# Optimization experiments

Hardware: AMD Instinct MI355X
Metric: run time of the kernel (lower is better)

The kernel has to match this reference:

```python
import jax, jax.numpy as jnp
import numpy as np

D_IN = 2048
D_OUT = 2048
NUM_HEADS = 16
NUM_KV_GROUPS = 4
GROUP_SIZE = NUM_HEADS // NUM_KV_GROUPS  # 4
HEAD_DIM = D_OUT // NUM_HEADS            # 128


def setup_inputs() -> dict:
    key = jax.random.key(0)
    ks = jax.random.split(key, 6)
    b, n = 2, 2048
    x = jax.random.normal(ks[0], (b, n, D_IN), dtype=jnp.float32)
    # weights stored as [in, out] so that x @ W matches torch's x @ weight.T
    Wq = jax.random.normal(ks[1], (D_IN, D_OUT), dtype=jnp.float32) * (1.0 / np.sqrt(D_IN))
    Wk = jax.random.normal(ks[2], (D_IN, NUM_KV_GROUPS * HEAD_DIM), dtype=jnp.float32) * (1.0 / np.sqrt(D_IN))
    Wv = jax.random.normal(ks[3], (D_IN, NUM_KV_GROUPS * HEAD_DIM), dtype=jnp.float32) * (1.0 / np.sqrt(D_IN))
    Wo = jax.random.normal(ks[4], (D_OUT, D_OUT), dtype=jnp.float32) * (1.0 / np.sqrt(D_OUT))
    bo = jax.random.normal(ks[5], (D_OUT,), dtype=jnp.float32) * 0.01
    return {"x": x, "Wq": Wq, "Wk": Wk, "Wv": Wv, "Wo": Wo, "bo": bo}


def reference(x, Wq, Wk, Wv, Wo, bo):
    b, n, _ = x.shape
    # projections
    q = (x @ Wq).reshape(b, n, NUM_KV_GROUPS, GROUP_SIZE, HEAD_DIM)  # [b,n,g,s,d]
    k = (x @ Wk).reshape(b, n, NUM_KV_GROUPS, HEAD_DIM)              # [b,n,g,d]
    v = (x @ Wv).reshape(b, n, NUM_KV_GROUPS, HEAD_DIM)
    scale = 1.0 / np.sqrt(HEAD_DIM).astype(np.float32)
    # scores: each group of GROUP_SIZE query heads shares one K/V head
    scores = jnp.einsum('bqgsd,bkgd->bgsqk', q, k) * scale  # [b,g,s,n,n]
    causal = jnp.arange(n)[:, None] < jnp.arange(n)[None, :]  # True above diagonal
    scores = jnp.where(causal, -jnp.inf, scores)
    attn = jax.nn.softmax(scores, axis=-1)
    # dropout omitted for determinism (eval-mode equivalent)
    ctx = jnp.einsum('bgsqk,bkgd->bqgsd', attn, v)  # [b,n,g,s,d]
    ctx = ctx.reshape(b, n, D_OUT)
    return ctx @ Wo + bo
```

## Files before the change

kernel.cpp:

```cpp
#include <hip/hip_runtime.h>
#include <hip/hip_bf16.h>

typedef short bf16x8 __attribute__((ext_vector_type(8)));
typedef float f32x4 __attribute__((ext_vector_type(4)));
typedef float f32x16 __attribute__((ext_vector_type(16)));
typedef unsigned int u32x4 __attribute__((ext_vector_type(4)));

#define MFMA16(a, b, c) __builtin_amdgcn_mfma_f32_16x16x32_bf16((a), (b), (c), 0, 0, 0)
#define MFMA32(a, b, c) __builtin_amdgcn_mfma_f32_32x32x16_bf16((a), (b), (c), 0, 0, 0)

static __device__ __forceinline__ unsigned short f2bf(float f) {
  union { float f; unsigned u; } v;
  v.f = f;
  unsigned r = (v.u + 0x7FFFu + ((v.u >> 16) & 1u)) >> 16;
  return (unsigned short)r;
}

static __device__ __forceinline__ unsigned pk2(float a, float b) {
  unsigned ua = __float_as_uint(a) + 0x8000u;
  unsigned ub = __float_as_uint(b) + 0x8000u;
  return (ua >> 16) | (ub & 0xFFFF0000u);
}

static __device__ __forceinline__ void gload16(const void* g, void* l) {
  __builtin_amdgcn_global_load_lds(
      (const __attribute__((address_space(1))) unsigned int*)g,
      (__attribute__((address_space(3))) unsigned int*)l, 16, 0, 0);
}

__global__ __launch_bounds__(256) void cast_f32_bf16(
    const float* __restrict__ src, unsigned short* __restrict__ dst, int n4) {
  int stride = gridDim.x * blockDim.x;
  for (int i = blockIdx.x * blockDim.x + threadIdx.x; i < n4; i += stride) {
    float4 v = reinterpret_cast<const float4*>(src)[i];
    ushort4 o;
    o.x = f2bf(v.x); o.y = f2bf(v.y); o.z = f2bf(v.z); o.w = f2bf(v.w);
    reinterpret_cast<ushort4*>(dst)[i] = o;
  }
}

__global__ __launch_bounds__(256) void prep_all(
    const float* __restrict__ Wq, const float* __restrict__ Wk,
    const float* __restrict__ Wv, const float* __restrict__ Wo,
    unsigned short* __restrict__ WqT, unsigned short* __restrict__ WkT,
    unsigned short* __restrict__ WvT, unsigned short* __restrict__ WoT) {
  __shared__ float tile[32][33];
  int id = blockIdx.x;
  const float* src; unsigned short* dst; int R, C, bx, by;
  if (id < 4096)      { src = Wq; dst = WqT; R = 2048; C = 2048; bx = id & 63; by = id >> 6; }
  else if (id < 5120) { id -= 4096; src = Wk; dst = WkT; R = 2048; C = 512; bx = id & 15; by = id >> 4; }
  else if (id < 6144) { id -= 5120; src = Wv; dst = WvT; R = 2048; C = 512; bx = id & 15; by = id >> 4; }
  else                { id -= 6144; src = Wo; dst = WoT; R = 2048; C = 2048; bx = id & 63; by = id >> 6; }
  int tx = threadIdx.x & 31;
  int ty = threadIdx.x >> 5;
  int r0 = by * 32, c0 = bx * 32;
#pragma unroll
  for (int i = 0; i < 32; i += 8)
    tile[ty + i][tx] = src[(size_t)(r0 + ty + i) * C + (c0 + tx)];
  __syncthreads();
#pragma unroll
  for (int i = 0; i < 32; i += 8)
    dst[(size_t)(c0 + ty + i) * R + (r0 + tx)] = f2bf(tile[tx][ty + i]);
}

template <int EPI>
static __device__ __forceinline__ void g8p_core(
    const unsigned short* __restrict__ A, const unsigned short* __restrict__ B,
    unsigned short* __restrict__ Cb, unsigned short* __restrict__ Cb2,
    float* __restrict__ Cf, const float* __restrict__ bias,
    int N, int K, int bid, unsigned short* Al, unsigned short* Bl) {
  const int tid = threadIdx.x;
  const int wave = tid >> 6, lane = tid & 63;
  const int l15 = lane & 15, l4 = lane >> 4;
  const int tilesN = N >> 7;
  const int bm = bid / tilesN, bn = bid % tilesN;
  const int row0 = bm << 8, col0 = bn << 7;
  const int wr = (wave >> 1) << 6;
  const int wc = (wave & 1) << 6;

  const unsigned short* sA[4];
  const unsigned short* sB[2];
#pragma unroll
  for (int i = 0; i < 4; ++i) {
    int q = i * 512 + wave * 64 + lane;
    int r = q >> 3, c = (q & 7) ^ (r & 7);
    sA[i] = A + (size_t)(row0 + r) * K + c * 8;
  }
#pragma unroll
  for (int i = 0; i < 2; ++i) {
    int q = i * 512 + wave * 64 + lane;
    int r = q >> 3, c = (q & 7) ^ (r & 7);
    sB[i] = B + (size_t)(col0 + r) * K + c * 8;
  }

#define STG_H1(t_, bi)                                                      \
  { const size_t ko = (size_t)(t_) * 64;                                    \
    gload16(sA[0] + ko, &Al[(bi)*16384 + (0 * 512 + wave * 64) * 8]);       \
    gload16(sA[1] + ko, &Al[(bi)*16384 + (1 * 512 + wave * 64) * 8]);       \
    gload16(sB[0] + ko, &Bl[(bi)*8192 + (0 * 512 + wave * 64) * 8]); }
#define STG_H2(t_, bi)                                                      \
  { const size_t ko = (size_t)(t_) * 64;                                    \
    gload16(sA[2] + ko, &Al[(bi)*16384 + (2 * 512 + wave * 64) * 8]);       \
    gload16(sA[3] + ko, &Al[(bi)*16384 + (3 * 512 + wave * 64) * 8]);       \
    gload16(sB[1] + ko, &Bl[(bi)*8192 + (1 * 512 + wave * 64) * 8]); }

  const int sw = l15 & 7;
  const int c0 = (l4 ^ sw) << 4;
  const int c1 = ((4 + l4) ^ sw) << 4;
  const int rbA = (wr + l15) << 7;
  const int rbB = (wc + l15) << 7;

  f32x4 acc[4][4] = {};
  const int NT = K >> 6;

  STG_H1(0, 0); STG_H2(0, 0);
  STG_H1(1, 1); STG_H2(1, 1);

  int cur = 0;
  for (int t = 0; t < NT; ++t) {
    int sb = cur + 2; if (sb >= 3) sb -= 3;
    if (t + 1 < NT) { asm volatile("s_waitcnt vmcnt(6)" ::: "memory"); }
    else            { asm volatile("s_waitcnt vmcnt(0)" ::: "memory"); }
    __builtin_amdgcn_s_barrier();
    asm volatile("" ::: "memory");
    const char* Ab = (const char*)&Al[cur * 16384];
    const char* Bb = (const char*)&Bl[cur * 8192];
    bf16x8 b0[4], b1[4], aA[2][2], aB[2][2];
#pragma unroll
    for (int n = 0; n < 4; ++n) {
      b0[n] = *(const bf16x8*)(Bb + rbB + n * 2048 + c0);
      b1[n] = *(const bf16x8*)(Bb + rbB + n * 2048 + c1);
    }
#pragma unroll
    for (int m = 0; m < 2; ++m) {
      aA[m][0] = *(const bf16x8*)(Ab + rbA + m * 2048 + c0);
      aA[m][1] = *(const bf16x8*)(Ab + rbA + m * 2048 + c1);
    }
    if (t + 2 < NT) STG_H1(t + 2, sb);
    asm volatile("" ::: "memory");
    __builtin_amdgcn_s_barrier();
    asm volatile("" ::: "memory");
    __builtin_amdgcn_s_setprio(1);
#pragma unroll
    for (int m = 0; m < 2; ++m)
#pragma unroll
      for (int n = 0; n < 4; ++n) {
        acc[m][n] = MFMA16(aA[m][0], b0[n], acc[m][n]);
        acc[m][n] = MFMA16(aA[m][1], b1[n], acc[m][n]);
      }
    __builtin_amdgcn_s_setprio(0);
#pragma unroll
    for (int m = 0; m < 2; ++m) {
      aB[m][0] = *(const bf16x8*)(Ab + rbA + (m + 2) * 2048 + c0);
      aB[m][1] = *(const bf16x8*)(Ab + rbA + (m + 2) * 2048 + c1);
    }
    if (t + 2 < NT) STG_H2(t + 2, sb);
    asm volatile("" ::: "memory");
    __builtin_amdgcn_s_barrier();
    asm volatile("" ::: "memory");
    __builtin_amdgcn_s_setprio(1);
#pragma unroll
    for (int m = 0; m < 2; ++m)
#pragma unroll
      for (int n = 0; n < 4; ++n) {
        acc[m + 2][n] = MFMA16(aB[m][0], b0[n], acc[m + 2][n]);
        acc[m + 2][n] = MFMA16(aB[m][1], b1[n], acc[m + 2][n]);
      }
    __builtin_amdgcn_s_setprio(0);
    cur += 1; if (cur >= 3) cur = 0;
  }
#undef STG_H1
#undef STG_H2

#pragma unroll
  for (int m = 0; m < 4; ++m) {
#pragma unroll
    for (int n = 0; n < 4; ++n) {
      int row = row0 + wr + m * 16 + l4 * 4;
      int col = col0 + wc + n * 16 + l15;
#pragma unroll
      for (int r = 0; r < 4; ++r) {
        if (EPI == 0) {
          Cb[(size_t)(row + r) * N + col] = f2bf(acc[m][n][r]);
        } else if (EPI == 1) {
          Cf[(size_t)(row + r) * N + col] = acc[m][n][r] + bias[col];
        } else {
          if (col < 2048) Cb[(size_t)(row + r) * 2048 + col] = f2bf(acc[m][n][r]);
          else            Cb2[(size_t)(row + r) * 512 + col - 2048] = f2bf(acc[m][n][r]);
        }
      }
    }
  }
}

__global__ __launch_bounds__(512, 2) void gemm8p_o(
    const unsigned short* __restrict__ A, const unsigned short* __restrict__ B,
    float* __restrict__ Cf, const float* __restrict__ bias, int N, int K) {
  __shared__ unsigned short Al[3 * 256 * 64];
  __shared__ unsigned short Bl[3 * 128 * 64];
  g8p_core<1>(A, B, nullptr, nullptr, Cf, bias, N, K, blockIdx.x, Al, Bl);
}

__global__ __launch_bounds__(512, 2) void gemm_fused3(
    const unsigned short* __restrict__ Xb, const unsigned short* __restrict__ Bqk,
    unsigned short* __restrict__ Qb, unsigned short* __restrict__ Kb,
    const unsigned short* __restrict__ WvT, unsigned short* __restrict__ VTb) {
  __shared__ unsigned short Al[3 * 256 * 64];
  __shared__ unsigned short Bl[3 * 128 * 64];
  if (blockIdx.x < 320)
    g8p_core<2>(Xb, Bqk, Qb, Kb, nullptr, nullptr, 2560, 2048, blockIdx.x, Al, Bl);
  else
    g8p_core<0>(WvT, Xb, VTb, nullptr, nullptr, nullptr, 4096, 2048, blockIdx.x - 320, Al, Bl);
}

__global__ __launch_bounds__(256, 2) void flash_gqa6(
    const unsigned short* __restrict__ Qb, const unsigned short* __restrict__ Kb,
    const unsigned short* __restrict__ VT, unsigned short* __restrict__ Ctx) {
  __shared__ unsigned short Sm[24576];

  const int tid = threadIdx.x;
  const int wave = tid >> 6, lane = tid & 63;
  const int l31 = lane & 31, hi = lane >> 5;
  const int i = blockIdx.x >> 3;
  const int bg = blockIdx.x & 7;
  const int qt = (i < 32) ? i : (95 - i);
  const int b = bg >> 2, g = bg & 3;
  const int h = (g << 2) | wave;
  const int q0 = qt << 5;
  const int T = qt + 1;

  bf16x8 qf[8];
  {
    const unsigned short* qp =
        Qb + (size_t)(b * 2048 + q0 + l31) * 2048 + h * 128 + hi * 8;
#pragma unroll
    for (int ds = 0; ds < 8; ++ds) qf[ds] = *(const bf16x8*)(qp + ds * 16);
  }

  const int rK0 = tid >> 4, cK = tid & 15, rK1 = rK0 + 16;
  const unsigned short* kSA =
      Kb + (size_t)(b * 2048 + rK0) * 512 + g * 128 + (cK ^ (rK0 & 7)) * 8;
  const unsigned short* kSB =
      Kb + (size_t)(b * 2048 + rK1) * 512 + g * 128 + (cK ^ (rK1 & 7)) * 8;
  const int cV = tid & 7;
  const unsigned short* vS[4];
#pragma unroll
  for (int c = 0; c < 4; ++c) {
    int row = c * 32 + (tid >> 3);
    vS[c] = VT + (size_t)(g * 128 + row) * 4096 + b * 2048 + (cV ^ (row & 7)) * 8;
  }

#define STAGE_K(t_, bi)                                           \
  {                                                               \
    unsigned short* kb_ = Sm + (bi)*4096;                         \
    const size_t ko_ = (size_t)(t_) * 32 * 512;                   \
    gload16(kSA + ko_, kb_ + wave * 512);                         \
    gload16(kSB + ko_, kb_ + 2048 + wave * 512);                  \
  }
#define STAGE_V(p_, bi, half)                                     \
  {                                                               \
    unsigned short* vb_ = Sm + 8192 + (bi)*8192;                  \
    const size_t po_ = (size_t)(p_) * 64;                         \
    const int c_ = (half)*2;                                      \
    gload16(vS[c_] + po_, vb_ + c_ * 2048 + wave * 512);          \
    gload16(vS[c_ + 1] + po_, vb_ + (c_ + 1) * 2048 + wave * 512);\
  }

  const float s2 = 0.12751744f;

  float m_r = -1e30f, l_r = 0.f;
  f32x16 o0 = {}, o1 = {}, o2 = {}, o3 = {};

  STAGE_K(0, 0);
  STAGE_V(0, 0, 0);
  STAGE_V(0, 0, 1);
  __syncthreads();

  for (int t = 0; t < T; ++t) {
    const int buf = t & 1;
    const int pb = (t >> 1) & 1;
    if (t + 1 < T) STAGE_K(t + 1, buf ^ 1);
    const int p1 = (t >> 1) + 1;
    if (2 * p1 < T) STAGE_V(p1, p1 & 1, t & 1);

    const char* Kl = (const char*)Sm + buf * 8192;
    const char* Vl = (const char*)Sm + 16384 + pb * 16384;
    const int kv = t << 5;
    f32x16 st = {};
    __builtin_amdgcn_s_setprio(1);
#pragma unroll
    for (int ds = 0; ds < 8; ++ds) {
      const int by = (l31 * 256 + ds * 32 + hi * 16) ^ ((l31 & 7) << 4);
      bf16x8 kf = *(const bf16x8*)(Kl + by);
      st = MFMA32(kf, qf[ds], st);
    }
    __builtin_amdgcn_s_setprio(0);
    if (t == qt) {
      const int q_abs = q0 + l31;
#pragma unroll
      for (int rr = 0; rr < 16; ++rr) {
        const int koff = (rr & 3) + 8 * (rr >> 2) + 4 * hi;
        st[rr] = (kv + koff <= q_abs) ? st[rr] * s2 : -1e30f;
      }
    } else {
#pragma unroll
      for (int rr = 0; rr < 16; ++rr) st[rr] *= s2;
    }
    float pm = st[0];
#pragma unroll
    for (int rr = 1; rr < 16; ++rr) pm = fmaxf(pm, st[rr]);
    pm = fmaxf(pm, __shfl_xor(pm, 32));
    if (!__all(pm - m_r <= 11.5f)) {
      const float mn = fmaxf(m_r, pm);
      const float osc = exp2f(m_r - mn);
      m_r = mn;
      l_r *= osc;
#pragma unroll
      for (int rr = 0; rr < 16; ++rr) {
        o0[rr] *= osc; o1[rr] *= osc; o2[rr] *= osc; o3[rr] *= osc;
      }
    }
    float ps = 0.f;
#pragma unroll
    for (int rr = 0; rr < 16; ++rr) { st[rr] = exp2f(st[rr] - m_r); ps += st[rr]; }
    ps += __shfl_xor(ps, 32);
    l_r += ps;
    unsigned w[8];
#pragma unroll
    for (int rp = 0; rp < 8; ++rp) w[rp] = pk2(st[2 * rp], st[2 * rp + 1]);
    __builtin_amdgcn_s_setprio(1);
#define PV_KS(ks)                                                             \
    {                                                                         \
      const int k4 = (ks)*4;                                                  \
      unsigned a0 = w[k4], a1 = w[k4 + 1], b0 = w[k4 + 2], b1 = w[k4 + 3];    \
      unsigned q0_ = hi ? a0 : b0, q1_ = hi ? a1 : b1;                        \
      unsigned e0 = (unsigned)__shfl_xor((int)q0_, 32);                       \
      unsigned e1 = (unsigned)__shfl_xor((int)q1_, 32);                       \
      union { u32x4 u; bf16x8 v; } pk;                                        \
      pk.u[0] = hi ? e0 : a0; pk.u[1] = hi ? e1 : a1;                         \
      pk.u[2] = hi ? b0 : e0; pk.u[3] = hi ? b1 : e1;                         \
      const int cb = (t & 1) * 64 + (ks)*32 + hi * 16;                        \
      { const int row = l31;      const int by = (row * 128 + cb) ^ ((row & 7) << 4); \
        bf16x8 vf = *(const bf16x8*)(Vl + by); o0 = MFMA32(vf, pk.v, o0); }   \
      { const int row = 32 + l31; const int by = (row * 128 + cb) ^ ((row & 7) << 4); \
        bf16x8 vf = *(const bf16x8*)(Vl + by); o1 = MFMA32(vf, pk.v, o1); }   \
      { const int row = 64 + l31; const int by = (row * 128 + cb) ^ ((row & 7) << 4); \
        bf16x8 vf = *(const bf16x8*)(Vl + by); o2 = MFMA32(vf, pk.v, o2); }   \
      { const int row = 96 + l31; const int by = (row * 128 + cb) ^ ((row & 7) << 4); \
        bf16x8 vf = *(const bf16x8*)(Vl + by); o3 = MFMA32(vf, pk.v, o3); }   \
    }
    PV_KS(0) PV_KS(1)
#undef PV_KS
    __builtin_amdgcn_s_setprio(0);
    __syncthreads();
  }
#undef STAGE_K
#undef STAGE_V

  const float inv = 1.f / l_r;
  unsigned short* cp = Ctx + (size_t)(b * 2048 + q0 + l31) * 2048 + h * 128;
#pragma unroll
  for (int a = 0; a < 4; ++a) {
    ushort4 p0, p1, p2, p3;
    p0.x = f2bf(o0[4 * a + 0] * inv); p0.y = f2bf(o0[4 * a + 1] * inv);
    p0.z = f2bf(o0[4 * a + 2] * inv); p0.w = f2bf(o0[4 * a + 3] * inv);
    p1.x = f2bf(o1[4 * a + 0] * inv); p1.y = f2bf(o1[4 * a + 1] * inv);
    p1.z = f2bf(o1[4 * a + 2] * inv); p1.w = f2bf(o1[4 * a + 3] * inv);
    p2.x = f2bf(o2[4 * a + 0] * inv); p2.y = f2bf(o2[4 * a + 1] * inv);
    p2.z = f2bf(o2[4 * a + 2] * inv); p2.w = f2bf(o2[4 * a + 3] * inv);
    p3.x = f2bf(o3[4 * a + 0] * inv); p3.y = f2bf(o3[4 * a + 1] * inv);
    p3.z = f2bf(o3[4 * a + 2] * inv); p3.w = f2bf(o3[4 * a + 3] * inv);
    const int cc = 8 * a + 4 * hi;
    *(ushort4*)(cp + 0 * 32 + cc) = p0;
    *(ushort4*)(cp + 1 * 32 + cc) = p1;
    *(ushort4*)(cp + 2 * 32 + cc) = p2;
    *(ushort4*)(cp + 3 * 32 + cc) = p3;
  }
}

extern "C" void kernel_launch(void* const* d_in, const int* in_sizes, int n_in,
                              void* d_out, int out_size, void* d_ws, size_t ws_size,
                              hipStream_t stream) {
  (void)in_sizes; (void)n_in; (void)out_size; (void)ws_size;
  const float* x  = (const float*)d_in[0];
  const float* Wq = (const float*)d_in[1];
  const float* Wk = (const float*)d_in[2];
  const float* Wv = (const float*)d_in[3];
  const float* Wo = (const float*)d_in[4];
  const float* bo = (const float*)d_in[5];
  float* out = (float*)d_out;

  unsigned short* Xb  = (unsigned short*)d_ws;
  unsigned short* WqT = Xb  + (size_t)4096 * 2048;
  unsigned short* WkT = WqT + (size_t)2048 * 2048;
  unsigned short* WvT = WkT + (size_t)512 * 2048;
  unsigned short* WoT = WvT + (size_t)512 * 2048;
  unsigned short* Qb  = WoT + (size_t)2048 * 2048;
  unsigned short* Kb  = Qb  + (size_t)4096 * 2048;
  unsigned short* VTb = Kb  + (size_t)4096 * 512;
  unsigned short* Ctx = VTb + (size_t)512 * 4096;

  cast_f32_bf16<<<2048, 256, 0, stream>>>(x, Xb, (4096 * 2048) / 4);
  prep_all<<<10240, 256, 0, stream>>>(Wq, Wk, Wv, Wo, WqT, WkT, WvT, WoT);

  gemm_fused3<<<dim3(384), 512, 0, stream>>>(Xb, WqT, Qb, Kb, WvT, VTb);

  flash_gqa6<<<dim3(512), 256, 0, stream>>>(Qb, Kb, VTb, Ctx);

  gemm8p_o<<<dim3(256), 512, 0, stream>>>(Ctx, WoT, out, bo, 2048, 2048);
}
```

Before: 209.8 us.

## Widen flash attention KV tile to 64 keys per iteration

The attention kernel now processes 64 keys per loop iteration instead of 32, staging K and V together into double-buffered LDS tiles of 64 rows. This halves the number of loop iterations, barriers and online-softmax rescale checks, and gives each iteration more independent MFMAs to overlap. In exchange LDS use grows from 48 KB to 64 KB per block, register pressure rises from the two score accumulators, and the diagonal tile may compute up to 32 fully masked keys.

```diff
diff --git a/kernel.cpp b/kernel.cpp
--- a/kernel.cpp
+++ b/kernel.cpp
@@ -213,10 +213,10 @@
     g8p_core<0>(WvT, Xb, VTb, nullptr, nullptr, nullptr, 4096, 2048, blockIdx.x - 320, Al, Bl);
 }
 
-__global__ __launch_bounds__(256, 2) void flash_gqa6(
+__global__ __launch_bounds__(256, 2) void flash_gqa7(
     const unsigned short* __restrict__ Qb, const unsigned short* __restrict__ Kb,
     const unsigned short* __restrict__ VT, unsigned short* __restrict__ Ctx) {
-  __shared__ unsigned short Sm[24576];
+  __shared__ unsigned short Sm[32768];
 
   const int tid = threadIdx.x;
   const int wave = tid >> 6, lane = tid & 63;
@@ -227,7 +227,7 @@
   const int b = bg >> 2, g = bg & 3;
   const int h = (g << 2) | wave;
   const int q0 = qt << 5;
-  const int T = qt + 1;
+  const int T = (qt >> 1) + 1;
 
   bf16x8 qf[8];
   {
@@ -237,78 +237,76 @@
     for (int ds = 0; ds < 8; ++ds) qf[ds] = *(const bf16x8*)(qp + ds * 16);
   }
 
-  const int rK0 = tid >> 4, cK = tid & 15, rK1 = rK0 + 16;
-  const unsigned short* kSA =
-      Kb + (size_t)(b * 2048 + rK0) * 512 + g * 128 + (cK ^ (rK0 & 7)) * 8;
-  const unsigned short* kSB =
-      Kb + (size_t)(b * 2048 + rK1) * 512 + g * 128 + (cK ^ (rK1 & 7)) * 8;
-  const int cV = tid & 7;
-  const unsigned short* vS[4];
-#pragma unroll
-  for (int c = 0; c < 4; ++c) {
-    int row = c * 32 + (tid >> 3);
-    vS[c] = VT + (size_t)(g * 128 + row) * 4096 + b * 2048 + (cV ^ (row & 7)) * 8;
-  }
-
-#define STAGE_K(t_, bi)                                           \
-  {                                                               \
-    unsigned short* kb_ = Sm + (bi)*4096;                         \
-    const size_t ko_ = (size_t)(t_) * 32 * 512;                   \
-    gload16(kSA + ko_, kb_ + wave * 512);                         \
-    gload16(kSB + ko_, kb_ + 2048 + wave * 512);                  \
-  }
-#define STAGE_V(p_, bi, half)                                     \
-  {                                                               \
-    unsigned short* vb_ = Sm + 8192 + (bi)*8192;                  \
-    const size_t po_ = (size_t)(p_) * 64;                         \
-    const int c_ = (half)*2;                                      \
-    gload16(vS[c_] + po_, vb_ + c_ * 2048 + wave * 512);          \
-    gload16(vS[c_ + 1] + po_, vb_ + (c_ + 1) * 2048 + wave * 512);\
+  const int cK = tid & 15, rK = tid >> 4;
+  const unsigned short* kS0 = Kb + (size_t)(b * 2048 + rK +  0) * 512 + g * 128 + (cK ^ ((rK +  0) & 7)) * 8;
+  const unsigned short* kS1 = Kb + (size_t)(b * 2048 + rK + 16) * 512 + g * 128 + (cK ^ ((rK + 16) & 7)) * 8;
+  const unsigned short* kS2 = Kb + (size_t)(b * 2048 + rK + 32) * 512 + g * 128 + (cK ^ ((rK + 32) & 7)) * 8;
+  const unsigned short* kS3 = Kb + (size_t)(b * 2048 + rK + 48) * 512 + g * 128 + (cK ^ ((rK + 48) & 7)) * 8;
+  const int cV = tid & 7, rV = tid >> 3;
+  const unsigned short* vS0 = VT + (size_t)(g * 128 + rV +  0) * 4096 + b * 2048 + (cV ^ ((rV +  0) & 7)) * 8;
+  const unsigned short* vS1 = VT + (size_t)(g * 128 + rV + 32) * 4096 + b * 2048 + (cV ^ ((rV + 32) & 7)) * 8;
+  const unsigned short* vS2 = VT + (size_t)(g * 128 + rV + 64) * 4096 + b * 2048 + (cV ^ ((rV + 64) & 7)) * 8;
+  const unsigned short* vS3 = VT + (size_t)(g * 128 + rV + 96) * 4096 + b * 2048 + (cV ^ ((rV + 96) & 7)) * 8;
+
+#define STAGE7(t_, bi)                                          \
+  {                                                             \
+    unsigned short* kb_ = Sm + (bi)*8192;                       \
+    unsigned short* vb_ = Sm + 16384 + (bi)*8192;               \
+    const size_t ko_ = (size_t)(t_) * 64 * 512;                 \
+    const size_t vo_ = (size_t)(t_) * 64;                       \
+    gload16(kS0 + ko_, kb_ + 0 * 2048 + wave * 512);            \
+    gload16(kS1 + ko_, kb_ + 1 * 2048 + wave * 512);            \
+    gload16(kS2 + ko_, kb_ + 2 * 2048 + wave * 512);            \
+    gload16(kS3 + ko_, kb_ + 3 * 2048 + wave * 512);            \
+    gload16(vS0 + vo_, vb_ + 0 * 2048 + wave * 512);            \
+    gload16(vS1 + vo_, vb_ + 1 * 2048 + wave * 512);            \
+    gload16(vS2 + vo_, vb_ + 2 * 2048 + wave * 512);            \
+    gload16(vS3 + vo_, vb_ + 3 * 2048 + wave * 512);            \
   }
 
   const float s2 = 0.12751744f;
-
   float m_r = -1e30f, l_r = 0.f;
   f32x16 o0 = {}, o1 = {}, o2 = {}, o3 = {};
 
-  STAGE_K(0, 0);
-  STAGE_V(0, 0, 0);
-  STAGE_V(0, 0, 1);
+  STAGE7(0, 0);
   __syncthreads();
 
   for (int t = 0; t < T; ++t) {
     const int buf = t & 1;
-    const int pb = (t >> 1) & 1;
-    if (t + 1 < T) STAGE_K(t + 1, buf ^ 1);
-    const int p1 = (t >> 1) + 1;
-    if (2 * p1 < T) STAGE_V(p1, p1 & 1, t & 1);
-
-    const char* Kl = (const char*)Sm + buf * 8192;
-    const char* Vl = (const char*)Sm + 16384 + pb * 16384;
-    const int kv = t << 5;
-    f32x16 st = {};
+    if (t + 1 < T) STAGE7(t + 1, buf ^ 1);
+    const char* Kl = (const char*)Sm + buf * 16384;
+    const char* Vl = (const char*)Sm + 32768 + buf * 16384;
+    const int kv = t << 6;
+    f32x16 st0 = {}, st1 = {};
     __builtin_amdgcn_s_setprio(1);
 #pragma unroll
     for (int ds = 0; ds < 8; ++ds) {
-      const int by = (l31 * 256 + ds * 32 + hi * 16) ^ ((l31 & 7) << 4);
-      bf16x8 kf = *(const bf16x8*)(Kl + by);
-      st = MFMA32(kf, qf[ds], st);
+      const int c = ds * 32 + hi * 16;
+      const int by0 = (l31 * 256 + c) ^ ((l31 & 7) << 4);
+      const int by1 = ((32 + l31) * 256 + c) ^ ((l31 & 7) << 4);
+      bf16x8 kf0 = *(const bf16x8*)(Kl + by0);
+      bf16x8 kf1 = *(const bf16x8*)(Kl + by1);
+      st0 = MFMA32(kf0, qf[ds], st0);
+      st1 = MFMA32(kf1, qf[ds], st1);
     }
     __builtin_amdgcn_s_setprio(0);
-    if (t == qt) {
-      const int q_abs = q0 + l31;
+    const int q_abs = q0 + l31;
+    if (kv + 64 > q0) {
 #pragma unroll
       for (int rr = 0; rr < 16; ++rr) {
         const int koff = (rr & 3) + 8 * (rr >> 2) + 4 * hi;
-        st[rr] = (kv + koff <= q_abs) ? st[rr] * s2 : -1e30f;
+        st0[rr] = (kv + koff <= q_abs) ? st0[rr] * s2 : -1e30f;
+        st1[rr] = (kv + 32 + koff <= q_abs) ? st1[rr] * s2 : -1e30f;
       }
     } else {
 #pragma unroll
-      for (int rr = 0; rr < 16; ++rr) st[rr] *= s2;
-    }
-    float pm = st[0];
-#pragma unroll
-    for (int rr = 1; rr < 16; ++rr) pm = fmaxf(pm, st[rr]);
+      for (int rr = 0; rr < 16; ++rr) { st0[rr] *= s2; st1[rr] *= s2; }
+    }
+    float pm = st0[0];
+#pragma unroll
+    for (int rr = 1; rr < 16; ++rr) pm = fmaxf(pm, st0[rr]);
+#pragma unroll
+    for (int rr = 0; rr < 16; ++rr) pm = fmaxf(pm, st1[rr]);
     pm = fmaxf(pm, __shfl_xor(pm, 32));
     if (!__all(pm - m_r <= 11.5f)) {
       const float mn = fmaxf(m_r, pm);
@@ -322,24 +320,29 @@
     }
     float ps = 0.f;
 #pragma unroll
-    for (int rr = 0; rr < 16; ++rr) { st[rr] = exp2f(st[rr] - m_r); ps += st[rr]; }
+    for (int rr = 0; rr < 16; ++rr) { st0[rr] = exp2f(st0[rr] - m_r); ps += st0[rr]; }
+#pragma unroll
+    for (int rr = 0; rr < 16; ++rr) { st1[rr] = exp2f(st1[rr] - m_r); ps += st1[rr]; }
     ps += __shfl_xor(ps, 32);
     l_r += ps;
-    unsigned w[8];
-#pragma unroll
-    for (int rp = 0; rp < 8; ++rp) w[rp] = pk2(st[2 * rp], st[2 * rp + 1]);
+    unsigned w0[8], w1[8];
+#pragma unroll
+    for (int rp = 0; rp < 8; ++rp) {
+      w0[rp] = pk2(st0[2 * rp], st0[2 * rp + 1]);
+      w1[rp] = pk2(st1[2 * rp], st1[2 * rp + 1]);
+    }
     __builtin_amdgcn_s_setprio(1);
-#define PV_KS(ks)                                                             \
+#define PV_KS(ks, W)                                                          \
     {                                                                         \
-      const int k4 = (ks)*4;                                                  \
-      unsigned a0 = w[k4], a1 = w[k4 + 1], b0 = w[k4 + 2], b1 = w[k4 + 3];    \
+      const int k4 = ((ks) & 1) * 4;                                          \
+      unsigned a0 = W[k4], a1 = W[k4 + 1], b0 = W[k4 + 2], b1 = W[k4 + 3];    \
       unsigned q0_ = hi ? a0 : b0, q1_ = hi ? a1 : b1;                        \
       unsigned e0 = (unsigned)__shfl_xor((int)q0_, 32);                       \
       unsigned e1 = (unsigned)__shfl_xor((int)q1_, 32);                       \
       union { u32x4 u; bf16x8 v; } pk;                                        \
       pk.u[0] = hi ? e0 : a0; pk.u[1] = hi ? e1 : a1;                         \
       pk.u[2] = hi ? b0 : e0; pk.u[3] = hi ? b1 : e1;                         \
-      const int cb = (t & 1) * 64 + (ks)*32 + hi * 16;                        \
+      const int cb = (ks)*32 + hi * 16;                                       \
       { const int row = l31;      const int by = (row * 128 + cb) ^ ((row & 7) << 4); \
         bf16x8 vf = *(const bf16x8*)(Vl + by); o0 = MFMA32(vf, pk.v, o0); }   \
       { const int row = 32 + l31; const int by = (row * 128 + cb) ^ ((row & 7) << 4); \
@@ -349,13 +352,12 @@
       { const int row = 96 + l31; const int by = (row * 128 + cb) ^ ((row & 7) << 4); \
         bf16x8 vf = *(const bf16x8*)(Vl + by); o3 = MFMA32(vf, pk.v, o3); }   \
     }
-    PV_KS(0) PV_KS(1)
+    PV_KS(0, w0) PV_KS(1, w0) PV_KS(2, w1) PV_KS(3, w1)
 #undef PV_KS
     __builtin_amdgcn_s_setprio(0);
     __syncthreads();
   }
-#undef STAGE_K
-#undef STAGE_V
+#undef STAGE7
 
   const float inv = 1.f / l_r;
   unsigned short* cp = Ctx + (size_t)(b * 2048 + q0 + l31) * 2048 + h * 128;
@@ -405,7 +407,7 @@
 
   gemm_fused3<<<dim3(384), 512, 0, stream>>>(Xb, WqT, Qb, Kb, WvT, VTb);
 
-  flash_gqa6<<<dim3(512), 256, 0, stream>>>(Qb, Kb, VTb, Ctx);
+  flash_gqa7<<<dim3(512), 256, 0, stream>>>(Qb, Kb, VTb, Ctx);
 
   gemm8p_o<<<dim3(256), 512, 0, stream>>>(Ctx, WoT, out, bo, 2048, 2048);
 }
```

After: 197.3 us. -5.9%, faster.

## Split KV range across two wave groups in flash attention with LDS merge

Applied to the files above, without the earlier changes.

The attention block grows from 4 to 8 waves. Each head now has two waves that handle alternating 32-key tiles (split-K over the KV sequence), and both stage a 64-key K/V chunk per iteration into a larger double-buffered shared memory. At the end, the second wave's partial output, max and sum go through LDS and are merged with the first wave's state using log-sum-exp rescaling. The goal is to halve the serial loop length per block and add more waves for latency hiding, at the cost of more LDS, a final merge step and idle waves on the odd tile of the diagonal.

```diff
diff --git a/kernel.cpp b/kernel.cpp
--- a/kernel.cpp
+++ b/kernel.cpp
@@ -213,10 +213,10 @@
     g8p_core<0>(WvT, Xb, VTb, nullptr, nullptr, nullptr, 4096, 2048, blockIdx.x - 320, Al, Bl);
 }
 
-__global__ __launch_bounds__(256, 2) void flash_gqa6(
+__global__ __launch_bounds__(512, 4) void flash_gqa8(
     const unsigned short* __restrict__ Qb, const unsigned short* __restrict__ Kb,
     const unsigned short* __restrict__ VT, unsigned short* __restrict__ Ctx) {
-  __shared__ unsigned short Sm[24576];
+  __shared__ unsigned short Sm[34816];
 
   const int tid = threadIdx.x;
   const int wave = tid >> 6, lane = tid & 63;
@@ -225,9 +225,11 @@
   const int bg = blockIdx.x & 7;
   const int qt = (i < 32) ? i : (95 - i);
   const int b = bg >> 2, g = bg & 3;
-  const int h = (g << 2) | wave;
+  const int hl = wave & 3;
+  const int h = (g << 2) | hl;
+  const int part = wave >> 2;
   const int q0 = qt << 5;
-  const int T = qt + 1;
+  const int R = (qt >> 1) + 1;
 
   bf16x8 qf[8];
   {
@@ -237,144 +239,169 @@
     for (int ds = 0; ds < 8; ++ds) qf[ds] = *(const bf16x8*)(qp + ds * 16);
   }
 
-  const int rK0 = tid >> 4, cK = tid & 15, rK1 = rK0 + 16;
-  const unsigned short* kSA =
-      Kb + (size_t)(b * 2048 + rK0) * 512 + g * 128 + (cK ^ (rK0 & 7)) * 8;
-  const unsigned short* kSB =
-      Kb + (size_t)(b * 2048 + rK1) * 512 + g * 128 + (cK ^ (rK1 & 7)) * 8;
-  const int cV = tid & 7;
-  const unsigned short* vS[4];
-#pragma unroll
-  for (int c = 0; c < 4; ++c) {
-    int row = c * 32 + (tid >> 3);
-    vS[c] = VT + (size_t)(g * 128 + row) * 4096 + b * 2048 + (cV ^ (row & 7)) * 8;
-  }
-
-#define STAGE_K(t_, bi)                                           \
-  {                                                               \
-    unsigned short* kb_ = Sm + (bi)*4096;                         \
-    const size_t ko_ = (size_t)(t_) * 32 * 512;                   \
-    gload16(kSA + ko_, kb_ + wave * 512);                         \
-    gload16(kSB + ko_, kb_ + 2048 + wave * 512);                  \
-  }
-#define STAGE_V(p_, bi, half)                                     \
-  {                                                               \
-    unsigned short* vb_ = Sm + 8192 + (bi)*8192;                  \
-    const size_t po_ = (size_t)(p_) * 64;                         \
-    const int c_ = (half)*2;                                      \
-    gload16(vS[c_] + po_, vb_ + c_ * 2048 + wave * 512);          \
-    gload16(vS[c_ + 1] + po_, vb_ + (c_ + 1) * 2048 + wave * 512);\
+  const int rK = tid >> 4, cK = tid & 15;
+  const unsigned short* kS =
+      Kb + (size_t)(b * 2048 + rK) * 512 + g * 128 + (cK ^ (rK & 7)) * 8;
+  const int rV = tid >> 3, cV = tid & 7;
+  const unsigned short* vSa =
+      VT + (size_t)(g * 128 + rV) * 4096 + b * 2048 + (cV ^ (rV & 7)) * 8;
+  const int rVb = rV + 64;
+  const unsigned short* vSb =
+      VT + (size_t)(g * 128 + rVb) * 4096 + b * 2048 + (cV ^ (rVb & 7)) * 8;
+
+#define STAGE8(r_, bi)                                                   \
+  {                                                                      \
+    unsigned short* base_ = Sm + (bi)*16384;                             \
+    const int t0_ = 2 * (r_);                                            \
+    gload16(kS + (size_t)t0_ * 16384, base_ + wave * 512);               \
+    if (t0_ + 1 <= qt)                                                   \
+      gload16(kS + (size_t)(t0_ + 1) * 16384, base_ + 4096 + wave * 512);\
+    const size_t vo_ = (size_t)(r_) * 64;                                \
+    gload16(vSa + vo_, base_ + 8192 + wave * 512);                       \
+    gload16(vSb + vo_, base_ + 12288 + wave * 512);                      \
   }
 
   const float s2 = 0.12751744f;
-
   float m_r = -1e30f, l_r = 0.f;
   f32x16 o0 = {}, o1 = {}, o2 = {}, o3 = {};
 
-  STAGE_K(0, 0);
-  STAGE_V(0, 0, 0);
-  STAGE_V(0, 0, 1);
+  STAGE8(0, 0);
   __syncthreads();
 
-  for (int t = 0; t < T; ++t) {
-    const int buf = t & 1;
-    const int pb = (t >> 1) & 1;
-    if (t + 1 < T) STAGE_K(t + 1, buf ^ 1);
-    const int p1 = (t >> 1) + 1;
-    if (2 * p1 < T) STAGE_V(p1, p1 & 1, t & 1);
-
-    const char* Kl = (const char*)Sm + buf * 8192;
-    const char* Vl = (const char*)Sm + 16384 + pb * 16384;
-    const int kv = t << 5;
-    f32x16 st = {};
-    __builtin_amdgcn_s_setprio(1);
-#pragma unroll
-    for (int ds = 0; ds < 8; ++ds) {
-      const int by = (l31 * 256 + ds * 32 + hi * 16) ^ ((l31 & 7) << 4);
-      bf16x8 kf = *(const bf16x8*)(Kl + by);
-      st = MFMA32(kf, qf[ds], st);
-    }
-    __builtin_amdgcn_s_setprio(0);
-    if (t == qt) {
-      const int q_abs = q0 + l31;
-#pragma unroll
-      for (int rr = 0; rr < 16; ++rr) {
-        const int koff = (rr & 3) + 8 * (rr >> 2) + 4 * hi;
-        st[rr] = (kv + koff <= q_abs) ? st[rr] * s2 : -1e30f;
-      }
-    } else {
-#pragma unroll
-      for (int rr = 0; rr < 16; ++rr) st[rr] *= s2;
-    }
-    float pm = st[0];
-#pragma unroll
-    for (int rr = 1; rr < 16; ++rr) pm = fmaxf(pm, st[rr]);
-    pm = fmaxf(pm, __shfl_xor(pm, 32));
-    if (!__all(pm - m_r <= 11.5f)) {
-      const float mn = fmaxf(m_r, pm);
-      const float osc = exp2f(m_r - mn);
-      m_r = mn;
-      l_r *= osc;
-#pragma unroll
-      for (int rr = 0; rr < 16; ++rr) {
-        o0[rr] *= osc; o1[rr] *= osc; o2[rr] *= osc; o3[rr] *= osc;
-      }
-    }
-    float ps = 0.f;
-#pragma unroll
-    for (int rr = 0; rr < 16; ++rr) { st[rr] = exp2f(st[rr] - m_r); ps += st[rr]; }
-    ps += __shfl_xor(ps, 32);
-    l_r += ps;
-    unsigned w[8];
-#pragma unroll
-    for (int rp = 0; rp < 8; ++rp) w[rp] = pk2(st[2 * rp], st[2 * rp + 1]);
-    __builtin_amdgcn_s_setprio(1);
+  for (int r = 0; r < R; ++r) {
+    const int buf = r & 1;
+    if (r + 1 < R) STAGE8(r + 1, buf ^ 1);
+    const int t32 = 2 * r + part;
+    if (t32 <= qt) {
+      const char* Kl = (const char*)Sm + buf * 32768 + part * 8192;
+      const char* Vl = (const char*)Sm + buf * 32768 + 16384;
+      const int kv = t32 << 5;
+      f32x16 st = {};
+      __builtin_amdgcn_s_setprio(1);
+#pragma unroll
+      for (int ds = 0; ds < 8; ++ds) {
+        const int by = (l31 * 256 + ds * 32 + hi * 16) ^ ((l31 & 7) << 4);
+        bf16x8 kf = *(const bf16x8*)(Kl + by);
+        st = MFMA32(kf, qf[ds], st);
+      }
+      __builtin_amdgcn_s_setprio(0);
+      if (t32 == qt) {
+        const int q_abs = q0 + l31;
+#pragma unroll
+        for (int rr = 0; rr < 16; ++rr) {
+          const int koff = (rr & 3) + 8 * (rr >> 2) + 4 * hi;
+          st[rr] = (kv + koff <= q_abs) ? st[rr] * s2 : -1e30f;
+        }
+      } else {
+#pragma unroll
+        for (int rr = 0; rr < 16; ++rr) st[rr] *= s2;
+      }
+      float pm = st[0];
+#pragma unroll
+      for (int rr = 1; rr < 16; ++rr) pm = fmaxf(pm, st[rr]);
+      pm = fmaxf(pm, __shfl_xor(pm, 32));
+      if (!__all(pm - m_r <= 11.5f)) {
+        const float mn = fmaxf(m_r, pm);
+        const float osc = exp2f(m_r - mn);
+        m_r = mn;
+        l_r *= osc;
+#pragma unroll
+        for (int rr = 0; rr < 16; ++rr) {
+          o0[rr] *= osc; o1[rr] *= osc; o2[rr] *= osc; o3[rr] *= osc;
+        }
+      }
+      float ps = 0.f;
+#pragma unroll
+      for (int rr = 0; rr < 16; ++rr) { st[rr] = exp2f(st[rr] - m_r); ps += st[rr]; }
+      ps += __shfl_xor(ps, 32);
+      l_r += ps;
+      unsigned w[8];
+#pragma unroll
+      for (int rp = 0; rp < 8; ++rp) w[rp] = pk2(st[2 * rp], st[2 * rp + 1]);
+      __builtin_amdgcn_s_setprio(1);
 #define PV_KS(ks)                                                             \
-    {                                                                         \
-      const int k4 = (ks)*4;                                                  \
-      unsigned a0 = w[k4], a1 = w[k4 + 1], b0 = w[k4 + 2], b1 = w[k4 + 3];    \
-      unsigned q0_ = hi ? a0 : b0, q1_ = hi ? a1 : b1;                        \
-      unsigned e0 = (unsigned)__shfl_xor((int)q0_, 32);                       \
-      unsigned e1 = (unsigned)__shfl_xor((int)q1_, 32);                       \
-      union { u32x4 u; bf16x8 v; } pk;                                        \
-      pk.u[0] = hi ? e0 : a0; pk.u[1] = hi ? e1 : a1;                         \
-      pk.u[2] = hi ? b0 : e0; pk.u[3] = hi ? b1 : e1;                         \
-      const int cb = (t & 1) * 64 + (ks)*32 + hi * 16;                        \
-      { const int row = l31;      const int by = (row * 128 + cb) ^ ((row & 7) << 4); \
-        bf16x8 vf = *(const bf16x8*)(Vl + by); o0 = MFMA32(vf, pk.v, o0); }   \
-      { const int row = 32 + l31; const int by = (row * 128 + cb) ^ ((row & 7) << 4); \
-        bf16x8 vf = *(const bf16x8*)(Vl + by); o1 = MFMA32(vf, pk.v, o1); }   \
-      { const int row = 64 + l31; const int by = (row * 128 + cb) ^ ((row & 7) << 4); \
-        bf16x8 vf = *(const bf16x8*)(Vl + by); o2 = MFMA32(vf, pk.v, o2); }   \
-      { const int row = 96 + l31; const int by = (row * 128 + cb) ^ ((row & 7) << 4); \
-        bf16x8 vf = *(const bf16x8*)(Vl + by); o3 = MFMA32(vf, pk.v, o3); }   \
-    }
-    PV_KS(0) PV_KS(1)
+      {                                                                       \
+        const int k4 = (ks)*4;                                                \
+        unsigned a0 = w[k4], a1 = w[k4 + 1], b0 = w[k4 + 2], b1 = w[k4 + 3];  \
+        unsigned q0_ = hi ? a0 : b0, q1_ = hi ? a1 : b1;                      \
+        unsigned e0 = (unsigned)__shfl_xor((int)q0_, 32);                     \
+        unsigned e1 = (unsigned)__shfl_xor((int)q1_, 32);                     \
+        union { u32x4 u; bf16x8 v; } pk;                                      \
+        pk.u[0] = hi ? e0 : a0; pk.u[1] = hi ? e1 : a1;                       \
+        pk.u[2] = hi ? b0 : e0; pk.u[3] = hi ? b1 : e1;                       \
+        const int cb = part * 64 + (ks)*32 + hi * 16;                         \
+        { const int row = l31;      const int by = (row * 128 + cb) ^ ((row & 7) << 4); \
+          bf16x8 vf = *(const bf16x8*)(Vl + by); o0 = MFMA32(vf, pk.v, o0); } \
+        { const int row = 32 + l31; const int by = (row * 128 + cb) ^ ((row & 7) << 4); \
+          bf16x8 vf = *(const bf16x8*)(Vl + by); o1 = MFMA32(vf, pk.v, o1); } \
+        { const int row = 64 + l31; const int by = (row * 128 + cb) ^ ((row & 7) << 4); \
+          bf16x8 vf = *(const bf16x8*)(Vl + by); o2 = MFMA32(vf, pk.v, o2); } \
+        { const int row = 96 + l31; const int by = (row * 128 + cb) ^ ((row & 7) << 4); \
+          bf16x8 vf = *(const bf16x8*)(Vl + by); o3 = MFMA32(vf, pk.v, o3); } \
+      }
+      PV_KS(0) PV_KS(1)
 #undef PV_KS
-    __builtin_amdgcn_s_setprio(0);
+      __builtin_amdgcn_s_setprio(0);
+    }
     __syncthreads();
   }
-#undef STAGE_K
-#undef STAGE_V
-
-  const float inv = 1.f / l_r;
-  unsigned short* cp = Ctx + (size_t)(b * 2048 + q0 + l31) * 2048 + h * 128;
-#pragma unroll
-  for (int a = 0; a < 4; ++a) {
-    ushort4 p0, p1, p2, p3;
-    p0.x = f2bf(o0[4 * a + 0] * inv); p0.y = f2bf(o0[4 * a + 1] * inv);
-    p0.z = f2bf(o0[4 * a + 2] * inv); p0.w = f2bf(o0[4 * a + 3] * inv);
-    p1.x = f2bf(o1[4 * a + 0] * inv); p1.y = f2bf(o1[4 * a + 1] * inv);
-    p1.z = f2bf(o1[4 * a + 2] * inv); p1.w = f2bf(o1[4 * a + 3] * inv);
-    p2.x = f2bf(o2[4 * a + 0] * inv); p2.y = f2bf(o2[4 * a + 1] * inv);
-    p2.z = f2bf(o2[4 * a + 2] * inv); p2.w = f2bf(o2[4 * a + 3] * inv);
-    p3.x = f2bf(o3[4 * a + 0] * inv); p3.y = f2bf(o3[4 * a + 1] * inv);
-    p3.z = f2bf(o3[4 * a + 2] * inv); p3.w = f2bf(o3[4 * a + 3] * inv);
-    const int cc = 8 * a + 4 * hi;
-    *(ushort4*)(cp + 0 * 32 + cc) = p0;
-    *(ushort4*)(cp + 1 * 32 + cc) = p1;
-    *(ushort4*)(cp + 2 * 32 + cc) = p2;
-    *(ushort4*)(cp + 3 * 32 + cc) = p3;
+#undef STAGE8
+
+  float* F = (float*)Sm;
+  float* sc = F + (size_t)hl * 4352 + lane * 68;
+  if (part == 1) {
+    union { f32x16 v; f32x4 q[4]; } u;
+    u.v = o0;
+#pragma unroll
+    for (int k = 0; k < 4; ++k) *(f32x4*)(sc + 0 + 4 * k) = u.q[k];
+    u.v = o1;
+#pragma unroll
+    for (int k = 0; k < 4; ++k) *(f32x4*)(sc + 16 + 4 * k) = u.q[k];
+    u.v = o2;
+#pragma unroll
+    for (int k = 0; k < 4; ++k) *(f32x4*)(sc + 32 + 4 * k) = u.q[k];
+    u.v = o3;
+#pragma unroll
+    for (int k = 0; k < 4; ++k) *(f32x4*)(sc + 48 + 4 * k) = u.q[k];
+    sc[64] = m_r;
+    sc[65] = l_r;
+  }
+  __syncthreads();
+  if (part == 0) {
+    const float m2 = sc[64], l2 = sc[65];
+    const float mm = fmaxf(m_r, m2);
+    const float fa = exp2f(m_r - mm), fb = exp2f(m2 - mm);
+    const float inv = 1.f / (l_r * fa + l2 * fb);
+    unsigned short* cp = Ctx + (size_t)(b * 2048 + q0 + l31) * 2048 + h * 128;
+#pragma unroll
+    for (int a = 0; a < 4; ++a) {
+      f32x4 u0 = *(const f32x4*)(sc + 0 + 4 * a);
+      f32x4 u1 = *(const f32x4*)(sc + 16 + 4 * a);
+      f32x4 u2 = *(const f32x4*)(sc + 32 + 4 * a);
+      f32x4 u3 = *(const f32x4*)(sc + 48 + 4 * a);
+      ushort4 p0, p1, p2, p3;
+      p0.x = f2bf((o0[4 * a + 0] * fa + u0[0] * fb) * inv);
+      p0.y = f2bf((o0[4 * a + 1] * fa + u0[1] * fb) * inv);
+      p0.z = f2bf((o0[4 * a + 2] * fa + u0[2] * fb) * inv);
+      p0.w = f2bf((o0[4 * a + 3] * fa + u0[3] * fb) * inv);
+      p1.x = f2bf((o1[4 * a + 0] * fa + u1[0] * fb) * inv);
+      p1.y = f2bf((o1[4 * a + 1] * fa + u1[1] * fb) * inv);
+      p1.z = f2bf((o1[4 * a + 2] * fa + u1[2] * fb) * inv);
+      p1.w = f2bf((o1[4 * a + 3] * fa + u1[3] * fb) * inv);
+      p2.x = f2bf((o2[4 * a + 0] * fa + u2[0] * fb) * inv);
+      p2.y = f2bf((o2[4 * a + 1] * fa + u2[1] * fb) * inv);
+      p2.z = f2bf((o2[4 * a + 2] * fa + u2[2] * fb) * inv);
+      p2.w = f2bf((o2[4 * a + 3] * fa + u2[3] * fb) * inv);
+      p3.x = f2bf((o3[4 * a + 0] * fa + u3[0] * fb) * inv);
+      p3.y = f2bf((o3[4 * a + 1] * fa + u3[1] * fb) * inv);
+      p3.z = f2bf((o3[4 * a + 2] * fa + u3[2] * fb) * inv);
+      p3.w = f2bf((o3[4 * a + 3] * fa + u3[3] * fb) * inv);
+      const int cc = 8 * a + 4 * hi;
+      *(ushort4*)(cp + 0 * 32 + cc) = p0;
+      *(ushort4*)(cp + 1 * 32 + cc) = p1;
+      *(ushort4*)(cp + 2 * 32 + cc) = p2;
+      *(ushort4*)(cp + 3 * 32 + cc) = p3;
+    }
   }
 }
 
@@ -405,7 +432,7 @@
 
   gemm_fused3<<<dim3(384), 512, 0, stream>>>(Xb, WqT, Qb, Kb, WvT, VTb);
 
-  flash_gqa6<<<dim3(512), 256, 0, stream>>>(Qb, Kb, VTb, Ctx);
+  flash_gqa8<<<dim3(512), 512, 0, stream>>>(Qb, Kb, VTb, Ctx);
 
   gemm8p_o<<<dim3(256), 512, 0, stream>>>(Ctx, WoT, out, bo, 2048, 2048);
 }
```

Measured after the change: 298.1 us. 42.1% more time.
